# Kernel tuning notes

Hardware: AMD Instinct MI355X
Metric: run time of the kernel (lower is better)

Reference implementation:

```python
import jax, jax.numpy as jnp
import numpy as np

N = 768  # length of time vector

def setup_inputs() -> dict:
    key = jax.random.key(0)
    ks = jax.random.split(key, 4)
    # time vector (sorted grid-like values, as in a GP time axis)
    x = jnp.sort(jax.random.uniform(ks[0], (N,), dtype=jnp.float32) * (6 * np.pi))
    # MLP params: Linear(2,1024) -> Sigmoid -> Linear(1024,128) -> ReLU -> Linear(128,1)
    W1 = jax.random.normal(ks[1], (1024, 2), dtype=jnp.float32) * (1.0 / np.sqrt(2.0))
    b1 = jnp.zeros((1024,), dtype=jnp.float32)
    W2 = jax.random.normal(ks[2], (128, 1024), dtype=jnp.float32) * (1.0 / np.sqrt(1024.0))
    b2 = jnp.zeros((128,), dtype=jnp.float32)
    W3 = jax.random.normal(ks[3], (1, 128), dtype=jnp.float32) * (1.0 / np.sqrt(128.0))
    b3 = jnp.zeros((1,), dtype=jnp.float32)
    return {"x": x, "W1": W1, "b1": b1, "W2": W2, "b2": b2, "W3": W3, "b3": b3}


def reference(x, W1, b1, W2, b2, W3, b3):
    n = x.shape[0]
    # all (i, j) with j >= i  -> n(n+1)/2 pairs; replaces the Python double loop
    iu, ju = jnp.triu_indices(n)
    pairs = jnp.stack([x[iu], x[ju]], axis=-1)            # [P, 2]
    h = jax.nn.sigmoid(pairs @ W1.T + b1)                 # [P, 1024]
    h = jax.nn.relu(h @ W2.T + b2)                        # [P, 128]
    v = (h @ W3.T + b3)[:, 0]                             # [P]
    # K starts as eye; upper triangle INCLUDING diagonal is overwritten
    K = jnp.eye(n, dtype=x.dtype).at[iu, ju].set(v)       # [n, n] upper-triangular
    return K.T @ K                                        # symmetric PSD covariance
```

## Files before the change

### kernel.cpp

```cpp
#include <hip/hip_runtime.h>
#include <hip/hip_bf16.h>

#define NN 768
#define MD 1024
#define NPAIR 295296
#define NPBLK2 2307

typedef __attribute__((ext_vector_type(8))) short s16x8;
typedef __attribute__((ext_vector_type(4))) float f32x4;
typedef __attribute__((ext_vector_type(2))) float f32x2;
typedef __attribute__((ext_vector_type(2))) __bf16 b16x2;

__device__ __forceinline__ ushort bf16_rn(float f) {
    uint u = __builtin_bit_cast(uint, f);
    u += 0x7FFFu + ((u >> 16) & 1u);
    return (ushort)(u >> 16);
}

__device__ __forceinline__ void ptoij(int p, int& io, int& jo) {
    const float disc = (float)(1537 * 1537 - 8 * p);
    int i = (int)((1537.0f - sqrtf(disc)) * 0.5f);
    i = i < 0 ? 0 : (i > 767 ? 767 : i);
    while (i > 0 && p < i * (1537 - i) / 2) --i;
    while (i < 767 && p >= (i + 1) * (1536 - i) / 2) ++i;
    io = i;
    jo = i + (p - i * (1537 - i) / 2);
}

#define GLOAD16(gsrc, ldst)                                                        \
    __builtin_amdgcn_global_load_lds(                                              \
        (const __attribute__((address_space(1))) void*)(gsrc),                     \
        (__attribute__((address_space(3))) void*)(ldst), 16, 0, 0)

__global__ __launch_bounds__(256) void prep_all(
    const float* __restrict__ x,  const float* __restrict__ W1,
    const float* __restrict__ b1, const float* __restrict__ W2,
    ushort* __restrict__ WF, ushort* __restrict__ ECF,
    float* __restrict__ EAg)
{
    const int b = blockIdx.x;
    const float NL2E = -1.4426950408889634f;
    if (b < 64) {
        const int id = b * 256 + threadIdx.x;
        const int lane = id & 63;
        const int f = id >> 6;
        const int tn = f & 7;
        const int ks = (f >> 3) & 1;
        const int c  = f >> 4;
        const int k = tn * 16 + (lane & 15);
        const int m = c * 64 + ks * 32 + (lane >> 4) * 8;
        const float4 a = *reinterpret_cast<const float4*>(W2 + k * MD + m);
        const float4 bb = *reinterpret_cast<const float4*>(W2 + k * MD + m + 4);
        const float w[8] = {a.x, a.y, a.z, a.w, bb.x, bb.y, bb.z, bb.w};
        s16x8 h;
#pragma unroll
        for (int e = 0; e < 8; ++e) h[e] = (short)bf16_rn(w[e]);
        *reinterpret_cast<s16x8*>(WF + id * 8) = h;
    } else if (b < 448) {
        const int id = (b - 64) * 256 + threadIdx.x;
        const int j = id >> 7;
        const int m8 = id & 127;
        const float xj = x[j];
        const int mbase = m8 * 8;
        s16x8 h;
#pragma unroll
        for (int e = 0; e < 8; ++e) {
            const float cm = W1[(mbase + e) * 2 + 1];
            h[e] = (short)bf16_rn(__builtin_amdgcn_exp2f(cm * xj * NL2E));
        }
        const int c    = mbase >> 6;
        const int ks   = (mbase >> 5) & 1;
        const int l4   = (mbase & 31) >> 3;
        const int lane = l4 * 16 + (j & 15);
        const int off  = (j >> 4) * 16384 + c * 1024 + ks * 512 + lane * 8;
        *reinterpret_cast<s16x8*>(ECF + off) = h;
    } else {
        const int id = (b - 448) * 256 + threadIdx.x;
        const int i = id >> 10;
        const int m = id & 1023;
        const float2 w = reinterpret_cast<const float2*>(W1)[m];
        EAg[id] = __builtin_amdgcn_exp2f(fmaf(w.x, x[i], b1[m]) * NL2E);
    }
}

#define LOADB_T(cc, ks)                                                      \
    {                                                                        \
        const ushort* wb_ = WF + (cc) * 8192 + (ks) * 4096 + lane * 8;       \
        _Pragma("unroll")                                                    \
        for (int tn_ = 0; tn_ < 8; ++tn_)                                    \
            bh[tn_] = *reinterpret_cast<const s16x8*>(wb_ + tn_ * 512);      \
    }

#define LOADEC(cc, ks, dst)                                                  \
    {                                                                        \
        const ushort* e_ = ECF + jg0 * 16384 + (cc) * 1024 + (ks) * 512 + lane * 8; \
        dst[0] = *reinterpret_cast<const s16x8*>(e_);                        \
        dst[1] = *reinterpret_cast<const s16x8*>(e_ + 16384);                \
    }

#define SIG_T(cc, ks_, ec)                                                   \
    {                                                                        \
        const int m0_ = (cc) * 64 + (ks_) * 32 + l4 * 8;                     \
        const f32x4 ea0_ = *reinterpret_cast<const f32x4*>(&EAl[m0_]);       \
        const f32x4 ea1_ = *reinterpret_cast<const f32x4*>(&EAl[m0_ + 4]);   \
        _Pragma("unroll")                                                    \
        for (int tm_ = 0; tm_ < 2; ++tm_) {                                  \
            union { s16x8 v; uint u[4]; } ec_;                               \
            ec_.v = ec[tm_];                                                 \
            union { s16x8 v; uint u[4]; } fr_;                               \
            _Pragma("unroll")                                                \
            for (int h_ = 0; h_ < 4; ++h_) {                                 \
                const uint uu_ = ec_.u[h_];                                  \
                const float el_ = __builtin_bit_cast(float, uu_ << 16);      \
                const float eh_ = __builtin_bit_cast(float, uu_ & 0xFFFF0000u); \
                const float ga_ = (h_ < 2) ? ea0_[2 * h_] : ea1_[2 * h_ - 4];     \
                const float gb_ = (h_ < 2) ? ea0_[2 * h_ + 1] : ea1_[2 * h_ - 3]; \
                const float t0_ = fmaf(el_, ga_, 1.0f);                      \
                const float t1_ = fmaf(eh_, gb_, 1.0f);                      \
                b16x2 p_;                                                    \
                p_.x = (__bf16)__builtin_amdgcn_rcpf(t0_);                   \
                p_.y = (__bf16)__builtin_amdgcn_rcpf(t1_);                   \
                fr_.u[h_] = __builtin_bit_cast(uint, p_);                    \
            }                                                                \
            ah[tm_] = fr_.v;                                                 \
        }                                                                    \
    }

#define MFMA_T()                                                             \
    {                                                                        \
        __builtin_amdgcn_s_setprio(1);                                       \
        _Pragma("unroll")                                                    \
        for (int tm_ = 0; tm_ < 2; ++tm_)                                    \
            _Pragma("unroll")                                                \
            for (int tn_ = 0; tn_ < 8; ++tn_)                                \
                acc[tm_][tn_] = __builtin_amdgcn_mfma_f32_16x16x32_bf16(     \
                    ah[tm_], bh[tn_], acc[tm_][tn_], 0, 0, 0);               \
        __builtin_amdgcn_s_setprio(0);                                       \
    }

__global__ __launch_bounds__(256, 3) void mlp_tab(
    const float* __restrict__ EAg, const ushort* __restrict__ ECF,
    const ushort* __restrict__ WF,
    const float* __restrict__ b2, const float* __restrict__ W3,
    const float* __restrict__ b3, float* __restrict__ K)
{
    const int i  = blockIdx.y;
    const int j0 = blockIdx.x * 128;
    if (j0 + 127 < i) return;

    __shared__ __align__(16) float EAl[MD];

    const int t = threadIdx.x;
    const int lane = t & 63, wv = t >> 6;
    const int l15 = lane & 15, l4 = lane >> 4;

    const int jw  = j0 + wv * 32;
    const int jg0 = jw >> 4;

    GLOAD16(EAg + i * MD + wv * 256 + lane * 4, (char*)EAl + wv * 1024);

    f32x4 acc[2][8];
#pragma unroll
    for (int a = 0; a < 2; ++a)
#pragma unroll
        for (int b = 0; b < 8; ++b) acc[a][b] = (f32x4){0.f, 0.f, 0.f, 0.f};

    s16x8 bh[8], ecA[2], ecB[2], ah[2];
    LOADB_T(0, 0);
    LOADEC(0, 0, ecA);
    __syncthreads();

    for (int c = 0; c < 16; ++c) {
        LOADEC(c, 1, ecB);
        SIG_T(c, 0, ecA);
        MFMA_T();
        LOADB_T(c, 1);
        if (c < 15) LOADEC(c + 1, 0, ecA);
        SIG_T(c, 1, ecB);
        MFMA_T();
        if (c < 15) LOADB_T(c + 1, 0);
    }

    float w3v[8], b2v[8];
#pragma unroll
    for (int tn = 0; tn < 8; ++tn) {
        const int k = tn * 16 + l15;
        w3v[tn] = W3[k];
        b2v[tn] = b2[k];
    }
    const float b3v = b3[0];
#pragma unroll
    for (int tm = 0; tm < 2; ++tm)
#pragma unroll
        for (int r = 0; r < 4; ++r) {
            float v = 0.f;
#pragma unroll
            for (int tn = 0; tn < 8; ++tn)
                v = fmaf(w3v[tn], fmaxf(acc[tm][tn][r] + b2v[tn], 0.f), v);
            v += __shfl_xor(v, 1, 16);
            v += __shfl_xor(v, 2, 16);
            v += __shfl_xor(v, 4, 16);
            v += __shfl_xor(v, 8, 16);
            if (l15 == 0) {
                const int j = jw + tm * 16 + l4 * 4 + r;
                if (j >= i) K[i * NN + j] = v + b3v;
            }
        }
}

__global__ __launch_bounds__(256) void w2frag(const float* __restrict__ W2,
                                              ushort* __restrict__ WF)
{
    const int id = blockIdx.x * 256 + threadIdx.x;
    const int lane = id & 63;
    const int f = id >> 6;
    const int tn = f & 7;
    const int ks = (f >> 3) & 1;
    const int c  = f >> 4;
    const int k = tn * 16 + (lane & 15);
    const int m = c * 64 + ks * 32 + (lane >> 4) * 8;
    const float4 a = *reinterpret_cast<const float4*>(W2 + k * MD + m);
    const float4 b = *reinterpret_cast<const float4*>(W2 + k * MD + m + 4);
    const float w[8] = {a.x, a.y, a.z, a.w, b.x, b.y, b.z, b.w};
    s16x8 h;
#pragma unroll
    for (int e = 0; e < 8; ++e) h[e] = (short)bf16_rn(w[e]);
    *reinterpret_cast<s16x8*>(WF + id * 8) = h;
}

#define LOADB(cc, ks)                                                        \
    {                                                                        \
        const ushort* wb_ = WF + (cc) * 8192 + (ks) * 4096 + lane * 8;       \
        _Pragma("unroll")                                                    \
        for (int tn_ = 0; tn_ < 8; ++tn_)                                    \
            bh[tn_] = *reinterpret_cast<const s16x8*>(wb_ + tn_ * 512);      \
    }

#define SIG_HALF(cc, ks_)                                                    \
    {                                                                        \
        const int m0_ = (cc) * 64 + (ks_) * 32 + l4 * 8;                     \
        const f32x4 a0_ = *reinterpret_cast<const f32x4*>(&sa[m0_]);         \
        const f32x4 a1_ = *reinterpret_cast<const f32x4*>(&sa[m0_ + 4]);     \
        const f32x4 c0_ = *reinterpret_cast<const f32x4*>(&sc[m0_]);         \
        const f32x4 c1_ = *reinterpret_cast<const f32x4*>(&sc[m0_ + 4]);     \
        const f32x4 b0_ = *reinterpret_cast<const f32x4*>(&sb[m0_]);         \
        const f32x4 b1_ = *reinterpret_cast<const f32x4*>(&sb[m0_ + 4]);     \
        _Pragma("unroll")                                                    \
        for (int tm_ = 0; tm_ < 2; ++tm_) {                                  \
            const f32x2 xi2_ = (f32x2){xia[tm_], xia[tm_]};                  \
            const f32x2 xj2_ = (f32x2){xja[tm_], xja[tm_]};                  \
            const f32x2 one2_ = (f32x2){1.f, 1.f};                           \
            union { s16x8 v; uint u[4]; } fr_;                               \
            _Pragma("unroll")                                                \
            for (int h_ = 0; h_ < 4; ++h_) {                                 \
                f32x2 av_, cv_, bv_;                                         \
                if (h_ < 2) {                                                \
                    av_ = (f32x2){a0_[2 * h_], a0_[2 * h_ + 1]};             \
                    cv_ = (f32x2){c0_[2 * h_], c0_[2 * h_ + 1]};             \
                    bv_ = (f32x2){b0_[2 * h_], b0_[2 * h_ + 1]};             \
                } else {                                                     \
                    av_ = (f32x2){a1_[2 * h_ - 4], a1_[2 * h_ - 3]};         \
                    cv_ = (f32x2){c1_[2 * h_ - 4], c1_[2 * h_ - 3]};         \
                    bv_ = (f32x2){b1_[2 * h_ - 4], b1_[2 * h_ - 3]};         \
                }                                                            \
                const f32x2 u2_ = __builtin_elementwise_fma(                 \
                    xi2_, av_, __builtin_elementwise_fma(xj2_, cv_, bv_));   \
                f32x2 e2_;                                                   \
                e2_[0] = __builtin_amdgcn_exp2f(u2_[0]);                     \
                e2_[1] = __builtin_amdgcn_exp2f(u2_[1]);                     \
                const f32x2 t2_ = e2_ + one2_;                               \
                b16x2 p_;                                                    \
                p_.x = (__bf16)__builtin_amdgcn_rcpf(t2_[0]);                \
                p_.y = (__bf16)__builtin_amdgcn_rcpf(t2_[1]);                \
                fr_.u[h_] = __builtin_bit_cast(uint, p_);                    \
            }                                                                \
            ah[tm_] = fr_.v;                                                 \
        }                                                                    \
    }

#define MFMA_HALF()                                                          \
    {                                                                        \
        __builtin_amdgcn_s_setprio(1);                                       \
        _Pragma("unroll")                                                    \
        for (int tm_ = 0; tm_ < 2; ++tm_)                                    \
            _Pragma("unroll")                                                \
            for (int tn_ = 0; tn_ < 8; ++tn_)                                \
                acc[tm_][tn_] = __builtin_amdgcn_mfma_f32_16x16x32_bf16(     \
                    ah[tm_], bh[tn_], acc[tm_][tn_], 0, 0, 0);               \
        __builtin_amdgcn_s_setprio(0);                                       \
    }

__global__ __launch_bounds__(256, 3) void mlp_pairs_reg(
    const float* __restrict__ x,
    const float* __restrict__ W1, const float* __restrict__ b1,
    const ushort* __restrict__ WF,
    const float* __restrict__ b2, const float* __restrict__ W3,
    const float* __restrict__ b3, float* __restrict__ K)
{
    __shared__ __align__(16) float sa[MD], sc[MD], sb[MD];

    const int t = threadIdx.x;
    const int lane = t & 63;
    const int l15 = lane & 15, l4 = lane >> 4;
    const int wv = t >> 6;

    const float NL2E = -1.4426950408889634f;
    for (int m = t; m < MD; m += 256) {
        const float2 w = reinterpret_cast<const float2*>(W1)[m];
        sa[m] = w.x * NL2E;
        sc[m] = w.y * NL2E;
        sb[m] = b1[m] * NL2E;
    }

    const int pairbase = blockIdx.x * 128 + wv * 32;

    float xia[2], xja[2];
#pragma unroll
    for (int tm = 0; tm < 2; ++tm) {
        const int p = pairbase + tm * 16 + l15;
        if (p < NPAIR) {
            int i, j;
            ptoij(p, i, j);
            xia[tm] = x[i];
            xja[tm] = x[j];
        } else {
            xia[tm] = 0.f;
            xja[tm] = 0.f;
        }
    }

    f32x4 acc[2][8];
#pragma unroll
    for (int a = 0; a < 2; ++a)
#pragma unroll
        for (int b = 0; b < 8; ++b) acc[a][b] = (f32x4){0.f, 0.f, 0.f, 0.f};

    s16x8 bh[8];
    LOADB(0, 0);
    __syncthreads();

    s16x8 ah[2];
    for (int c = 0; c < 16; ++c) {
        SIG_HALF(c, 0);
        MFMA_HALF();
        LOADB(c, 1);
        SIG_HALF(c, 1);
        MFMA_HALF();
        if (c < 15) LOADB(c + 1, 0);
    }

    float w3v[8], b2v[8];
#pragma unroll
    for (int tn = 0; tn < 8; ++tn) {
        const int k = tn * 16 + l15;
        w3v[tn] = W3[k];
        b2v[tn] = b2[k];
    }
    const float b3v = b3[0];
#pragma unroll
    for (int tm = 0; tm < 2; ++tm)
#pragma unroll
        for (int r = 0; r < 4; ++r) {
            float v = 0.f;
#pragma unroll
            for (int tn = 0; tn < 8; ++tn)
                v = fmaf(w3v[tn], fmaxf(acc[tm][tn][r] + b2v[tn], 0.f), v);
            v += __shfl_xor(v, 1, 16);
            v += __shfl_xor(v, 2, 16);
            v += __shfl_xor(v, 4, 16);
            v += __shfl_xor(v, 8, 16);
            if (l15 == 0) {
                const int p = pairbase + tm * 16 + l4 * 4 + r;
                if (p < NPAIR) {
                    int i, j;
                    ptoij(p, i, j);
                    K[i * NN + j] = v + b3v;
                }
            }
        }
}

__global__ __launch_bounds__(256) void ktk(const float* __restrict__ K,
                                           float* __restrict__ C)
{
    const int b0 = blockIdx.x * 64;
    const int a0 = blockIdx.y * 64;
    if (b0 < a0) return;
    __shared__ float Ka[64][68];
    __shared__ float Kb[64][68];
    const int t  = threadIdx.x;
    const int tb = t & 15;
    const int ta = t >> 4;
    float acc[4][4];
#pragma unroll
    for (int u = 0; u < 4; u++)
#pragma unroll
        for (int v = 0; v < 4; v++) acc[u][v] = 0.f;
    const int kmax = a0 + 64;
    for (int k0 = 0; k0 < kmax; k0 += 64) {
#pragma unroll
        for (int q = 0; q < 4; q++) {
            const int f  = t + q * 256;
            const int kk = f >> 4;
            const int c4 = (f & 15) * 4;
            *reinterpret_cast<float4*>(&Ka[kk][c4]) =
                *reinterpret_cast<const float4*>(K + (k0 + kk) * NN + a0 + c4);
            *reinterpret_cast<float4*>(&Kb[kk][c4]) =
                *reinterpret_cast<const float4*>(K + (k0 + kk) * NN + b0 + c4);
        }
        __syncthreads();
#pragma unroll 8
        for (int kk = 0; kk < 64; kk++) {
            const float4 av = *reinterpret_cast<const float4*>(&Ka[kk][ta * 4]);
            const float4 bv = *reinterpret_cast<const float4*>(&Kb[kk][tb * 4]);
            const float a4[4] = {av.x, av.y, av.z, av.w};
            const float b4[4] = {bv.x, bv.y, bv.z, bv.w};
#pragma unroll
            for (int u = 0; u < 4; u++)
#pragma unroll
                for (int v = 0; v < 4; v++)
                    acc[u][v] = fmaf(a4[u], b4[v], acc[u][v]);
        }
        __syncthreads();
    }
#pragma unroll
    for (int u = 0; u < 4; u++) {
        float4 o;
        o.x = acc[u][0]; o.y = acc[u][1]; o.z = acc[u][2]; o.w = acc[u][3];
        *reinterpret_cast<float4*>(C + (a0 + ta * 4 + u) * NN + b0 + tb * 4) = o;
    }
    if (b0 > a0) {
#pragma unroll
        for (int v = 0; v < 4; v++) {
            float4 o;
            o.x = acc[0][v]; o.y = acc[1][v]; o.z = acc[2][v]; o.w = acc[3][v];
            *reinterpret_cast<float4*>(C + (b0 + tb * 4 + v) * NN + a0 + ta * 4) = o;
        }
    }
}

extern "C" void kernel_launch(void* const* d_in, const int* in_sizes, int n_in,
                              void* d_out, int out_size, void* d_ws, size_t ws_size,
                              hipStream_t stream)
{
    const float* x  = (const float*)d_in[0];
    const float* W1 = (const float*)d_in[1];
    const float* b1 = (const float*)d_in[2];
    const float* W2 = (const float*)d_in[3];
    const float* b2 = (const float*)d_in[4];
    const float* W3 = (const float*)d_in[5];
    const float* b3 = (const float*)d_in[6];
    float* Kmat = (float*)d_ws;
    float* C    = (float*)d_out;

    const size_t kBytes  = (size_t)NN * NN * sizeof(float);
    const size_t wBytes  = 262144;
    const size_t eaB     = (size_t)NN * MD * sizeof(float);
    const size_t ecB     = (size_t)48 * 16384 * sizeof(ushort);
    const size_t needTab = kBytes + wBytes + eaB + ecB;
    const size_t needFB  = kBytes + wBytes;

    hipMemsetAsync(Kmat, 0, kBytes, stream);
    if (ws_size >= needTab) {
        ushort* WF  = (ushort*)((char*)d_ws + kBytes);
        float*  EAg = (float*)((char*)d_ws + kBytes + wBytes);
        ushort* ECF = (ushort*)((char*)d_ws + kBytes + wBytes + eaB);
        prep_all<<<3520, 256, 0, stream>>>(x, W1, b1, W2, WF, ECF, EAg);
        mlp_tab<<<dim3(6, NN), 256, 0, stream>>>(EAg, ECF, WF, b2, W3, b3, Kmat);
    } else if (ws_size >= needFB) {
        ushort* WF = (ushort*)((char*)d_ws + kBytes);
        w2frag<<<64, 256, 0, stream>>>(W2, WF);
        mlp_pairs_reg<<<NPBLK2, 256, 0, stream>>>(x, W1, b1, WF, b2, W3, b3, Kmat);
    }
    ktk<<<dim3(NN / 64, NN / 64), 256, 0, stream>>>(Kmat, C);
}
```

Baseline: 176.3 us.

## Halve MLP column tile to 64 and compute sigmoid row table in-kernel

The pair-MLP kernel now runs 128-thread blocks covering 64 columns instead of 256-thread blocks covering 128, launched on a 12×768 grid. Each block is half as wide, so less work is wasted on tiles that straddle the diagonal and are only partly inside the upper triangle. The per-row exp(W1·x_i + b1) table is now built directly in LDS by each block. This removes the global EAg buffer and the prep blocks that filled it. In exchange, every block repeats a small amount of exp work, and the B-fragment and EC loads are amortised over fewer columns per block.

```diff
diff --git a/kernel.cpp b/kernel.cpp
--- a/kernel.cpp
+++ b/kernel.cpp
@@ -27,16 +27,10 @@
     jo = i + (p - i * (1537 - i) / 2);
 }
 
-#define GLOAD16(gsrc, ldst)                                                        \
-    __builtin_amdgcn_global_load_lds(                                              \
-        (const __attribute__((address_space(1))) void*)(gsrc),                     \
-        (__attribute__((address_space(3))) void*)(ldst), 16, 0, 0)
-
 __global__ __launch_bounds__(256) void prep_all(
     const float* __restrict__ x,  const float* __restrict__ W1,
-    const float* __restrict__ b1, const float* __restrict__ W2,
-    ushort* __restrict__ WF, ushort* __restrict__ ECF,
-    float* __restrict__ EAg)
+    const float* __restrict__ W2,
+    ushort* __restrict__ WF, ushort* __restrict__ ECF)
 {
     const int b = blockIdx.x;
     const float NL2E = -1.4426950408889634f;
@@ -56,7 +50,7 @@
 #pragma unroll
         for (int e = 0; e < 8; ++e) h[e] = (short)bf16_rn(w[e]);
         *reinterpret_cast<s16x8*>(WF + id * 8) = h;
-    } else if (b < 448) {
+    } else {
         const int id = (b - 64) * 256 + threadIdx.x;
         const int j = id >> 7;
         const int m8 = id & 127;
@@ -74,12 +68,6 @@
         const int lane = l4 * 16 + (j & 15);
         const int off  = (j >> 4) * 16384 + c * 1024 + ks * 512 + lane * 8;
         *reinterpret_cast<s16x8*>(ECF + off) = h;
-    } else {
-        const int id = (b - 448) * 256 + threadIdx.x;
-        const int i = id >> 10;
-        const int m = id & 1023;
-        const float2 w = reinterpret_cast<const float2*>(W1)[m];
-        EAg[id] = __builtin_amdgcn_exp2f(fmaf(w.x, x[i], b1[m]) * NL2E);
     }
 }
 
@@ -138,15 +126,16 @@
         __builtin_amdgcn_s_setprio(0);                                       \
     }
 
-__global__ __launch_bounds__(256, 3) void mlp_tab(
-    const float* __restrict__ EAg, const ushort* __restrict__ ECF,
-    const ushort* __restrict__ WF,
+__global__ __launch_bounds__(128, 3) void mlp_tab64(
+    const float* __restrict__ x,
+    const float* __restrict__ W1, const float* __restrict__ b1,
+    const ushort* __restrict__ ECF, const ushort* __restrict__ WF,
     const float* __restrict__ b2, const float* __restrict__ W3,
     const float* __restrict__ b3, float* __restrict__ K)
 {
     const int i  = blockIdx.y;
-    const int j0 = blockIdx.x * 128;
-    if (j0 + 127 < i) return;
+    const int j0 = blockIdx.x * 64;
+    if (j0 + 63 < i) return;
 
     __shared__ __align__(16) float EAl[MD];
 
@@ -157,7 +146,12 @@
     const int jw  = j0 + wv * 32;
     const int jg0 = jw >> 4;
 
-    GLOAD16(EAg + i * MD + wv * 256 + lane * 4, (char*)EAl + wv * 1024);
+    const float NL2E = -1.4426950408889634f;
+    const float xi = x[i];
+    for (int m = t; m < MD; m += 128) {
+        const float2 w = reinterpret_cast<const float2*>(W1)[m];
+        EAl[m] = __builtin_amdgcn_exp2f(fmaf(w.x, xi, b1[m]) * NL2E);
+    }
 
     f32x4 acc[2][8];
 #pragma unroll
@@ -455,18 +449,17 @@
 
     const size_t kBytes  = (size_t)NN * NN * sizeof(float);
     const size_t wBytes  = 262144;
-    const size_t eaB     = (size_t)NN * MD * sizeof(float);
     const size_t ecB     = (size_t)48 * 16384 * sizeof(ushort);
-    const size_t needTab = kBytes + wBytes + eaB + ecB;
+    const size_t needTab = kBytes + wBytes + ecB;
     const size_t needFB  = kBytes + wBytes;
 
     hipMemsetAsync(Kmat, 0, kBytes, stream);
     if (ws_size >= needTab) {
         ushort* WF  = (ushort*)((char*)d_ws + kBytes);
-        float*  EAg = (float*)((char*)d_ws + kBytes + wBytes);
-        ushort* ECF = (ushort*)((char*)d_ws + kBytes + wBytes + eaB);
-        prep_all<<<3520, 256, 0, stream>>>(x, W1, b1, W2, WF, ECF, EAg);
-        mlp_tab<<<dim3(6, NN), 256, 0, stream>>>(EAg, ECF, WF, b2, W3, b3, Kmat);
+        ushort* ECF = (ushort*)((char*)d_ws + kBytes + wBytes);
+        prep_all<<<448, 256, 0, stream>>>(x, W1, W2, WF, ECF);
+        mlp_tab64<<<dim3(12, NN), 128, 0, stream>>>(x, W1, b1, ECF, WF,
+                                                    b2, W3, b3, Kmat);
     } else if (ws_size >= needFB) {
         ushort* WF = (ushort*)((char*)d_ws + kBytes);
         w2frag<<<64, 256, 0, stream>>>(W2, WF);
```

After: 172.9 us. No clear change (-1.9%).
